# Kernel optimization log

Measured on AMD Instinct MI355X. Metric: run time of the kernel, lower is better.

The kernel has to match this reference:

```python
import jax, jax.numpy as jnp
import numpy as np

EOS_TOKEN = 1


def setup_inputs() -> dict:
    key = jax.random.key(0)
    B, S, V = 8, 512, 32000
    k1, k2, k3 = jax.random.split(key, 3)
    # log-probabilities, as NLLLoss expects log-softmax inputs
    input = jax.nn.log_softmax(jax.random.normal(k1, (B, S, V), dtype=jnp.float32), axis=-1)
    # class ids in [2, V) so the only EOS (=1) tokens are the ones we plant
    target = jax.random.randint(k2, (B, S), 2, V, dtype=jnp.int64)
    eos_pos = jax.random.randint(k3, (B,), 1, S, dtype=jnp.int64)  # >=1 avoids div-by-zero
    target = target.at[jnp.arange(B), eos_pos].set(EOS_TOKEN)
    return {"input": input, "target": target}


def reference(input, target):
    # input: [B, S, V] log-probs; target: [B, S] int ids
    B, S, V = input.shape
    # first EOS index per sequence (argmax of bool returns first True)
    eos_idx = jnp.argmax(target == EOS_TOKEN, axis=1)            # [B]
    # mask tokens 0..eos_idx inclusive
    mask = jnp.arange(S)[None, :] <= eos_idx[:, None]            # [B, S]
    # gather log p(target) per token
    tok_logp = jnp.take_along_axis(input, target[:, :, None], axis=2)[..., 0]  # [B, S]
    # per-sequence summed NLL normalized by eos_idx (matches original: / sequence_length)
    per_seq = -jnp.sum(jnp.where(mask, tok_logp, jnp.zeros((), input.dtype)), axis=1)
    per_seq = per_seq / eos_idx.astype(input.dtype)              # [B]
    return jnp.sum(per_seq)
```

## Files before the change

### kernel.cpp

```cpp
#include <hip/hip_runtime.h>

#define EOS_TOKEN 1

__global__ __launch_bounds__(1024) void nll_fused_kernel(
    const float* __restrict__ input,
    const int*   __restrict__ target,
    float*       __restrict__ out,
    int B, int S, int V)
{
    const int tid = threadIdx.x;
    const int TOT = B * S;

    __shared__ int   s_eos[32];
    __shared__ float s_inv[32];
    __shared__ float s_wsum[16];

    if (tid < B) s_eos[tid] = S;
    __syncthreads();

    int tgt[4];
    int idxv[4];
    #pragma unroll
    for (int i = 0; i < 4; ++i) {
        const int idx = tid + i * 1024;
        idxv[i] = idx;
        tgt[i]  = (idx < TOT) ? target[idx] : 0;
        if (idx < TOT && tgt[i] == EOS_TOKEN)
            atomicMin(&s_eos[idx / S], idx % S);
    }
    __syncthreads();

    if (tid < B) s_inv[tid] = 1.0f / (float)s_eos[tid];
    __syncthreads();

    float acc = 0.0f;
    #pragma unroll
    for (int i = 0; i < 4; ++i) {
        const int idx = idxv[i];
        if (idx < TOT) {
            const int b = idx / S;
            const int s = idx % S;
            if (s <= s_eos[b]) {
                const float lp = input[(size_t)idx * (size_t)V + (size_t)tgt[i]];
                acc -= lp * s_inv[b];
            }
        }
    }

    #pragma unroll
    for (int off = 32; off > 0; off >>= 1)
        acc += __shfl_down(acc, off, 64);

    const int lane = tid & 63;
    const int wid  = tid >> 6;
    if (lane == 0) s_wsum[wid] = acc;
    __syncthreads();

    if (tid == 0) {
        float sum = 0.0f;
        #pragma unroll
        for (int w = 0; w < 16; ++w) sum += s_wsum[w];
        out[0] = sum;
    }
}

extern "C" void kernel_launch(void* const* d_in, const int* in_sizes, int n_in,
                              void* d_out, int out_size, void* d_ws, size_t ws_size,
                              hipStream_t stream)
{
    const float* input  = (const float*)d_in[0];
    const int*   target = (const int*)d_in[1];
    float*       out    = (float*)d_out;

    const int S  = 512;
    const int BS = in_sizes[1];
    const int B  = BS / S;
    const int V  = (int)((long long)in_sizes[0] / (long long)BS);

    nll_fused_kernel<<<1, 1024, 0, stream>>>(input, target, out, B, S, V);
}
```

Measured before the change: 11.29 us.

## Issue gathers before EOS reduction and vectorize target loads per thread

Each thread now owns four contiguous tokens, loads their targets with one int4 load, and issues all four log-prob gathers unconditionally before the EOS atomicMin and barrier. The gather latency overlaps the EOS search instead of waiting on it, and one barrier plus the shared inverse array are removed. The change assumes B*S equals 4096 and that S is a multiple of 4, since bounds checks were dropped, and it reads gathered values past EOS that are then discarded.

```diff
diff --git a/kernel.cpp b/kernel.cpp
--- a/kernel.cpp
+++ b/kernel.cpp
@@ -8,44 +8,37 @@
     float*       __restrict__ out,
     int B, int S, int V)
 {
-    const int tid = threadIdx.x;
-    const int TOT = B * S;
+    const int tid  = threadIdx.x;
+    const int base = tid * 4;
+    const int b    = base / S;
+    const int s0   = base - b * S;
 
     __shared__ int   s_eos[32];
-    __shared__ float s_inv[32];
     __shared__ float s_wsum[16];
 
     if (tid < B) s_eos[tid] = S;
     __syncthreads();
 
-    int tgt[4];
-    int idxv[4];
+    const int4 t4 = *reinterpret_cast<const int4*>(target + base);
+    const int tgt[4] = { t4.x, t4.y, t4.z, t4.w };
+
+    float lp[4];
     #pragma unroll
-    for (int i = 0; i < 4; ++i) {
-        const int idx = tid + i * 1024;
-        idxv[i] = idx;
-        tgt[i]  = (idx < TOT) ? target[idx] : 0;
-        if (idx < TOT && tgt[i] == EOS_TOKEN)
-            atomicMin(&s_eos[idx / S], idx % S);
-    }
+    for (int j = 0; j < 4; ++j)
+        lp[j] = input[((size_t)base + j) * (size_t)V + (size_t)tgt[j]];
+
+    #pragma unroll
+    for (int j = 0; j < 4; ++j)
+        if (tgt[j] == EOS_TOKEN) atomicMin(&s_eos[b], s0 + j);
     __syncthreads();
 
-    if (tid < B) s_inv[tid] = 1.0f / (float)s_eos[tid];
-    __syncthreads();
-
-    float acc = 0.0f;
+    const int   eos = s_eos[b];
+    const float inv = 1.0f / (float)eos;
+    float sum = 0.0f;
     #pragma unroll
-    for (int i = 0; i < 4; ++i) {
-        const int idx = idxv[i];
-        if (idx < TOT) {
-            const int b = idx / S;
-            const int s = idx % S;
-            if (s <= s_eos[b]) {
-                const float lp = input[(size_t)idx * (size_t)V + (size_t)tgt[i]];
-                acc -= lp * s_inv[b];
-            }
-        }
-    }
+    for (int j = 0; j < 4; ++j)
+        if (s0 + j <= eos) sum += lp[j];
+    float acc = -sum * inv;
 
     #pragma unroll
     for (int off = 32; off > 0; off >>= 1)
@@ -57,10 +50,10 @@
     __syncthreads();
 
     if (tid == 0) {
-        float sum = 0.0f;
+        float total = 0.0f;
         #pragma unroll
-        for (int w = 0; w < 16; ++w) sum += s_wsum[w];
-        out[0] = sum;
+        for (int w = 0; w < 16; ++w) total += s_wsum[w];
+        out[0] = total;
     }
 }
 
```

Measured after the change: 10.81 us. -4.2%, faster.
